# Optimization experiments

Measured on AMD Instinct MI355X. Metric: run time of the kernel, lower is better.

The kernel has to match this reference:

```python
import jax, jax.numpy as jnp
import numpy as np

N_POINTS = 200
LEVEL_DIM = 4
NUM_LEVELS = 3
RESOLUTIONS = (8, 16, 32)  # base_resolution=8, per-level scale 2
BATCH = 32768


def _sph_to_cart(theta, phi):
    st = jnp.sin(theta)
    return jnp.stack([st * jnp.cos(phi), st * jnp.sin(phi), jnp.cos(theta)], axis=-1)


def _sample_points(x):
    # x: [B,4] -> points on segment between two unit-sphere points: [B, N_POINTS, 3]
    p1 = _sph_to_cart(x[:, 0], x[:, 1])
    p2 = _sph_to_cart(x[:, 2], x[:, 3])
    t = jnp.linspace(0.0, 1.0, N_POINTS, dtype=x.dtype).reshape(1, N_POINTS, 1)
    return p1[:, None, :] + (p2 - p1)[:, None, :] * t


def _grid_interp(points, table, R):
    # points: [B,S,3] in [-1,1]; table: [(R+1)^3, D] dense grid. Trilinear interp.
    u = jnp.clip((points + 1.0) * 0.5, 0.0, 1.0) * R
    p0 = jnp.clip(jnp.floor(u).astype(jnp.int32), 0, R - 1)
    f = u - p0.astype(u.dtype)
    Rp1 = R + 1
    out = jnp.zeros(points.shape[:-1] + (table.shape[-1],), dtype=table.dtype)
    for c in range(8):  # fixed 8 trilinear corners
        off = np.array([(c >> 2) & 1, (c >> 1) & 1, c & 1], dtype=np.int32)
        idx = p0 + off
        lin = (idx[..., 0] * Rp1 + idx[..., 1]) * Rp1 + idx[..., 2]
        w = jnp.prod(jnp.where(off == 1, f, 1.0 - f), axis=-1)
        out = out + w[..., None] * table[lin]
    return out


def setup_inputs() -> dict:
    key = jax.random.key(0)
    ks = jax.random.split(key, 8)
    pi = 3.14159265
    x = jax.random.uniform(ks[0], (BATCH, 4), dtype=jnp.float32) * pi
    grid0 = jax.random.normal(ks[1], ((RESOLUTIONS[0] + 1) ** 3, LEVEL_DIM), jnp.float32) * 0.1
    grid1 = jax.random.normal(ks[2], ((RESOLUTIONS[1] + 1) ** 3, LEVEL_DIM), jnp.float32) * 0.1
    grid2 = jax.random.normal(ks[3], ((RESOLUTIONS[2] + 1) ** 3, LEVEL_DIM), jnp.float32) * 0.1
    w_label = jax.random.normal(ks[4], (NUM_LEVELS, 1), jnp.float32) * 0.5
    b_label = jnp.zeros((1,), jnp.float32)
    w_rgb = jax.random.normal(ks[5], (NUM_LEVELS * (LEVEL_DIM - 1), 3), jnp.float32) * 0.3
    b_rgb = jnp.zeros((3,), jnp.float32)
    return {"x": x, "grid0": grid0, "grid1": grid1, "grid2": grid2,
            "w_label": w_label, "b_label": b_label, "w_rgb": w_rgb, "b_rgb": b_rgb}


def reference(x, grid0, grid1, grid2, w_label, b_label, w_rgb, b_rgb):
    # torch wraps ray sampling in no_grad -> stop_gradient
    points = jax.lax.stop_gradient(_sample_points(x))  # [B,S,3]
    enc = jnp.concatenate(
        [_grid_interp(points, g, R) for g, R in zip((grid0, grid1, grid2), RESOLUTIONS)],
        axis=-1)  # [B,S,12]
    labels_in = enc[:, :, ::LEVEL_DIM]                      # [B,S,3]
    all_prob = jax.nn.sigmoid(labels_in @ w_label + b_label)  # [B,S,1]
    output_hits = jnp.max(all_prob, axis=1)                 # [B,1]
    mask = np.ones(NUM_LEVELS * LEVEL_DIM, dtype=bool)
    mask[::LEVEL_DIM] = False
    rgb_feats = enc[:, :, mask]                             # [B,S,9]
    hit = (all_prob > 0.5).astype(enc.dtype)
    idx_first = jnp.argmax(hit, axis=1)                     # [B,1] first sample with prob>0.5 (0 if none)
    idx3 = jnp.broadcast_to(idx_first[:, :, None], (rgb_feats.shape[0], 1, rgb_feats.shape[2]))
    gathered = jnp.take_along_axis(rgb_feats, idx3, axis=1)[:, 0, :]  # [B,9]
    output_rgb = jax.nn.sigmoid(gathered @ w_rgb + b_rgb)   # [B,3]
    return (output_hits, output_rgb)
```

## Files before the change

### kernel.cpp

```cpp
#include <hip/hip_runtime.h>
#include <math.h>

#define NPTS 200
#define L33   33
#define NLAT  35937
#define NPREP (NLAT * 4)

template<int R>
__device__ __forceinline__ float tri_label(const float* __restrict__ g,
                                           float ux, float uy, float uz) {
    constexpr int Rp1 = R + 1;
    constexpr int SX  = Rp1 * Rp1;
    int ix = min((int)ux, R - 1);
    int iy = min((int)uy, R - 1);
    int iz = min((int)uz, R - 1);
    float fx = ux - (float)ix, fy = uy - (float)iy, fz = uz - (float)iz;
    int b = (ix * Rp1 + iy) * Rp1 + iz;
    float v000 = g[4*b],            v001 = g[4*(b+1)];
    float v010 = g[4*(b+Rp1)],      v011 = g[4*(b+Rp1+1)];
    float v100 = g[4*(b+SX)],       v101 = g[4*(b+SX+1)];
    float v110 = g[4*(b+SX+Rp1)],   v111 = g[4*(b+SX+Rp1+1)];
    float c00 = fmaf(fz, v001 - v000, v000);
    float c01 = fmaf(fz, v011 - v010, v010);
    float c10 = fmaf(fz, v101 - v100, v100);
    float c11 = fmaf(fz, v111 - v110, v110);
    float c0  = fmaf(fy, c01 - c00, c00);
    float c1  = fmaf(fy, c11 - c10, c10);
    return fmaf(fx, c1 - c0, c0);
}

__global__ __launch_bounds__(256)
void prep_kernel(const float* __restrict__ g0, const float* __restrict__ g1,
                 const float* __restrict__ g2, const float* __restrict__ wl,
                 const float* __restrict__ bl, float* __restrict__ Pf) {
    int id = blockIdx.x * blockDim.x + threadIdx.x;
    if (id >= NPREP) return;
    int c  = id & 3;
    int jj = id >> 2;
    int ix = jj % L33;
    int r  = jj / L33;
    int iz = r % L33;
    int iy = r / L33;
    int jy = min(iy + (c >> 1), L33 - 1);
    int jz = min(iz + (c & 1),  L33 - 1);
    float fx = (float)ix, fy = (float)jy, fz = (float)jz;
    float L0 = tri_label<8 >(g0, fx * 0.25f, fy * 0.25f, fz * 0.25f);
    float L1 = tri_label<16>(g1, fx * 0.5f,  fy * 0.5f,  fz * 0.5f);
    float L2 = g2[4 * ((ix * L33 + jy) * L33 + jz)];
    Pf[id] = bl[0] + wl[0] * L0 + wl[1] * L1 + wl[2] * L2;
}

template<int R>
__device__ __forceinline__ void rgb_corner(const float* __restrict__ g,
                                           float cx, float cy, float cz,
                                           int dx, int dy, int dz,
                                           float* f3) {
    constexpr int Rp1 = R + 1;
    float ux = cx * (float)R, uy = cy * (float)R, uz = cz * (float)R;
    int ix = min((int)ux, R - 1);
    int iy = min((int)uy, R - 1);
    int iz = min((int)uz, R - 1);
    float fx = ux - (float)ix, fy = uy - (float)iy, fz = uz - (float)iz;
    int idx = ((ix + dx) * Rp1 + (iy + dy)) * Rp1 + (iz + dz);
    float w = (dx ? fx : 1.0f - fx) * (dy ? fy : 1.0f - fy) * (dz ? fz : 1.0f - fz);
    float4 v = *reinterpret_cast<const float4*>(g + 4 * idx);
    f3[0] = w * v.y;
    f3[1] = w * v.z;
    f3[2] = w * v.w;
}

__global__ __launch_bounds__(256, 4)
void rays_kernel(const float* __restrict__ x,
                 const float4* __restrict__ P,
                 const float* __restrict__ g0,
                 const float* __restrict__ g1,
                 const float* __restrict__ g2,
                 const float* __restrict__ wr,
                 const float* __restrict__ br,
                 float* __restrict__ out_hits,
                 float* __restrict__ out_rgb,
                 int n)
{
    const int tid = blockIdx.x * blockDim.x + threadIdx.x;
    const int ray = tid >> 4;
    const int sub = (int)(threadIdx.x & 15);
    if (ray >= n) return;

    const float th1 = x[ray * 4 + 0];
    const float ph1 = x[ray * 4 + 1];
    const float th2 = x[ray * 4 + 2];
    const float ph2 = x[ray * 4 + 3];
    float s1 = __sinf(th1), c1 = __cosf(th1);
    float s2 = __sinf(th2), c2 = __cosf(th2);
    float p1x = s1 * __cosf(ph1), p1y = s1 * __sinf(ph1), p1z = c1;
    float p2x = s2 * __cosf(ph2), p2y = s2 * __sinf(ph2), p2z = c2;
    const float dxr = p2x - p1x, dyr = p2y - p1y, dzr = p2z - p1z;

    const float inv = 1.0f / (float)(NPTS - 1);
    const float sc  = 16.0f * inv;

    const float bx = fmaf(p1x, 16.0f, 16.0f);
    const float by = fmaf(p1y, 16.0f, 16.0f);
    const float bz = fmaf(p1z, 16.0f, 16.0f);
    const float dux = dxr * sc, duy = dyr * sc, duz = dzr * sc;

    const float subf = (float)sub;
    float maxlogit = -INFINITY;
    unsigned hmask = 0u;

#define POINT_BODY(I)                                                          \
    {                                                                          \
        float tf = subf + (float)(16 * (I));             \
        float ux = fmaf(tf, dux, bx);                                          \
        float uy = fmaf(tf, duy, by);                                          \
        float uz = fmaf(tf, duz, bz);                                          \
        int ix = min((int)ux, 31);                                             \
        int iy = min((int)uy, 31);                                             \
        int iz = min((int)uz, 31);                                             \
        float fx = ux - (float)ix;                                             \
        float fy = uy - (float)iy;                                             \
        float fz = uz - (float)iz;                                             \
        int jj = (iy * L33 + iz) * L33 + ix;                                   \
        const float4* p = P + jj;                                              \
        float4 q0 = p[0];                                                      \
        float4 q1 = p[1];                                                      \
        float mx = fmaf(fx, q1.x - q0.x, q0.x);                                \
        float my = fmaf(fx, q1.y - q0.y, q0.y);                                \
        float mz = fmaf(fx, q1.z - q0.z, q0.z);                                \
        float mw = fmaf(fx, q1.w - q0.w, q0.w);                                \
        float r0 = fmaf(fz, my - mx, mx);                                      \
        float r1 = fmaf(fz, mw - mz, mz);                                      \
        float logit = fmaf(fy, r1 - r0, r0);                                   \
        maxlogit = fmaxf(maxlogit, logit);                                     \
        hmask |= (logit > 0.0f) ? (1u << (I)) : 0u;                            \
    }

#pragma unroll
    for (int i = 0; i < 12; ++i) POINT_BODY(i)
    if (sub < 8) POINT_BODY(12)
#undef POINT_BODY

    int fc = hmask ? (16 * __builtin_ctz(hmask) + sub) : NPTS;

#pragma unroll
    for (int m = 8; m >= 1; m >>= 1) {
        maxlogit = fmaxf(maxlogit, __shfl_xor(maxlogit, m, 64));
        fc = min(fc, __shfl_xor(fc, m, 64));
    }

    const int tsel = (fc >= NPTS) ? 0 : fc;
    {
        float tt = (float)tsel * inv;
        float px = fmaf(dxr, tt, p1x);
        float py = fmaf(dyr, tt, p1y);
        float pz = fmaf(dzr, tt, p1z);
        float cx = fminf(fmaxf(fmaf(px, 0.5f, 0.5f), 0.0f), 1.0f);
        float cy = fminf(fmaxf(fmaf(py, 0.5f, 0.5f), 0.0f), 1.0f);
        float cz = fminf(fmaxf(fmaf(pz, 0.5f, 0.5f), 0.0f), 1.0f);
        const int s8 = sub & 7;
        const int dx = (s8 >> 2) & 1, dy = (s8 >> 1) & 1, dz = s8 & 1;
        float feat[9];
        rgb_corner<8 >(g0, cx, cy, cz, dx, dy, dz, &feat[0]);
        rgb_corner<16>(g1, cx, cy, cz, dx, dy, dz, &feat[3]);
        rgb_corner<32>(g2, cx, cy, cz, dx, dy, dz, &feat[6]);
        float acc[3];
#pragma unroll
        for (int c = 0; c < 3; ++c) {
            float a = 0.0f;
#pragma unroll
            for (int f = 0; f < 9; ++f) a = fmaf(feat[f], wr[f * 3 + c], a);
            acc[c] = a;
        }
#pragma unroll
        for (int m = 4; m >= 1; m >>= 1) {
#pragma unroll
            for (int c = 0; c < 3; ++c)
                acc[c] += __shfl_xor(acc[c], m, 64);
        }
        if (sub == 0) {
            out_hits[ray] = 1.0f / (1.0f + __expf(-maxlogit));
#pragma unroll
            for (int c = 0; c < 3; ++c)
                out_rgb[ray * 3 + c] = 1.0f / (1.0f + __expf(-(acc[c] + br[c])));
        }
    }
}

extern "C" void kernel_launch(void* const* d_in, const int* in_sizes, int n_in,
                              void* d_out, int out_size, void* d_ws, size_t ws_size,
                              hipStream_t stream) {
    const float* x  = (const float*)d_in[0];
    const float* g0 = (const float*)d_in[1];
    const float* g1 = (const float*)d_in[2];
    const float* g2 = (const float*)d_in[3];
    const float* wl = (const float*)d_in[4];
    const float* bl = (const float*)d_in[5];
    const float* wr = (const float*)d_in[6];
    const float* br = (const float*)d_in[7];

    const int n = in_sizes[0] / 4;
    float* out_hits = (float*)d_out;
    float* out_rgb  = (float*)d_out + n;

    float* Pf = (float*)d_ws;

    prep_kernel<<<(NPREP + 255) / 256, 256, 0, stream>>>(g0, g1, g2, wl, bl, Pf);

    const int block = 256;
    const int grid = (n * 16 + block - 1) / block;
    rays_kernel<<<grid, block, 0, stream>>>(x, (const float4*)Pf, g0, g1, g2,
                                            wr, br, out_hits, out_rgb, n);
}
```

Baseline: 22.02 us.

## Pack per-cell label corners as bf16 with fp32 fallback near threshold

Replaces the two float4 loads per sample with one 16-byte load of all eight cell corners stored as bf16. A new pass builds a full fp32 label table, then a per-cell bf16 table and a global max-abs bound. Samples whose approximate logit falls within a tolerance band of zero are re-evaluated in fp32 to keep the first-hit index exact. This halves gather bandwidth per sample but adds an extra prep launch, an atomic, and a divergent fallback loop. The max logit (hence output_hits) is now taken from the bf16 values, so it is only approximate.

```diff
diff --git a/kernel.cpp b/kernel.cpp
--- a/kernel.cpp
+++ b/kernel.cpp
@@ -3,8 +3,12 @@
 
 #define NPTS 200
 #define L33   33
+#define L33SQ 1089
 #define NLAT  35937
-#define NPREP (NLAT * 4)
+#define NCELL 32768
+
+#define WS_T_OFF_BYTES   (NCELL * 16)
+#define WS_THR_OFF_BYTES (WS_T_OFF_BYTES + NLAT * 4)
 
 template<int R>
 __device__ __forceinline__ float tri_label(const float* __restrict__ g,
@@ -30,24 +34,56 @@
 }
 
 __global__ __launch_bounds__(256)
-void prep_kernel(const float* __restrict__ g0, const float* __restrict__ g1,
-                 const float* __restrict__ g2, const float* __restrict__ wl,
-                 const float* __restrict__ bl, float* __restrict__ Pf) {
-    int id = blockIdx.x * blockDim.x + threadIdx.x;
-    if (id >= NPREP) return;
-    int c  = id & 3;
-    int jj = id >> 2;
-    int ix = jj % L33;
-    int r  = jj / L33;
-    int iz = r % L33;
-    int iy = r / L33;
-    int jy = min(iy + (c >> 1), L33 - 1);
-    int jz = min(iz + (c & 1),  L33 - 1);
-    float fx = (float)ix, fy = (float)jy, fz = (float)jz;
+void prep1_kernel(const float* __restrict__ g0, const float* __restrict__ g1,
+                  const float* __restrict__ g2, const float* __restrict__ wl,
+                  const float* __restrict__ bl, float* __restrict__ T,
+                  unsigned* __restrict__ thrU) {
+    int i = blockIdx.x * blockDim.x + threadIdx.x;
+    if (i == 0) *thrU = 0u;
+    if (i >= NLAT) return;
+    int jz = i % L33;
+    int r  = i / L33;
+    int jy = r % L33;
+    int jx = r / L33;
+    float fx = (float)jx, fy = (float)jy, fz = (float)jz;
     float L0 = tri_label<8 >(g0, fx * 0.25f, fy * 0.25f, fz * 0.25f);
     float L1 = tri_label<16>(g1, fx * 0.5f,  fy * 0.5f,  fz * 0.5f);
-    float L2 = g2[4 * ((ix * L33 + jy) * L33 + jz)];
-    Pf[id] = bl[0] + wl[0] * L0 + wl[1] * L1 + wl[2] * L2;
+    float L2 = g2[4 * i];
+    T[i] = bl[0] + wl[0] * L0 + wl[1] * L1 + wl[2] * L2;
+}
+
+__device__ __forceinline__ unsigned bf16_rne(float v) {
+    unsigned u = __float_as_uint(v);
+    return u + 0x7fffu + ((u >> 16) & 1u);
+}
+
+__global__ __launch_bounds__(256)
+void prep2_kernel(const float* __restrict__ T, uint4* __restrict__ H,
+                  unsigned* __restrict__ thrU) {
+    int cell = blockIdx.x * blockDim.x + threadIdx.x;
+    int ix = cell & 31;
+    int iz = (cell >> 5) & 31;
+    int iy = cell >> 10;
+    int b = (ix * L33 + iy) * L33 + iz;
+    float v000 = T[b],              v001 = T[b + 1];
+    float v010 = T[b + L33],        v011 = T[b + L33 + 1];
+    float v100 = T[b + L33SQ],      v101 = T[b + L33SQ + 1];
+    float v110 = T[b + L33SQ + L33],v111 = T[b + L33SQ + L33 + 1];
+    uint4 o;
+    o.x = (bf16_rne(v000) >> 16) | (bf16_rne(v001) & 0xffff0000u);
+    o.y = (bf16_rne(v010) >> 16) | (bf16_rne(v011) & 0xffff0000u);
+    o.z = (bf16_rne(v100) >> 16) | (bf16_rne(v101) & 0xffff0000u);
+    o.w = (bf16_rne(v110) >> 16) | (bf16_rne(v111) & 0xffff0000u);
+    H[cell] = o;
+    float ma = fmaxf(fmaxf(fmaxf(fabsf(v000), fabsf(v001)),
+                           fmaxf(fabsf(v010), fabsf(v011))),
+                     fmaxf(fmaxf(fabsf(v100), fabsf(v101)),
+                           fmaxf(fabsf(v110), fabsf(v111))));
+#pragma unroll
+    for (int m = 32; m >= 1; m >>= 1)
+        ma = fmaxf(ma, __shfl_xor(ma, m, 64));
+    if ((threadIdx.x & 63) == 0)
+        atomicMax(thrU, __float_as_uint(ma));
 }
 
 template<int R>
@@ -71,7 +107,9 @@
 
 __global__ __launch_bounds__(256, 4)
 void rays_kernel(const float* __restrict__ x,
-                 const float4* __restrict__ P,
+                 const uint4* __restrict__ H,
+                 const float* __restrict__ T,
+                 const unsigned* __restrict__ thrU,
                  const float* __restrict__ g0,
                  const float* __restrict__ g1,
                  const float* __restrict__ g2,
@@ -86,6 +124,9 @@
     const int sub = (int)(threadIdx.x & 15);
     if (ray >= n) return;
 
+    const float maxAbs = __uint_as_float(*thrU);
+    const float thrG = fmaf(4e-3f, maxAbs, 1e-5f);
+
     const float th1 = x[ray * 4 + 0];
     const float ph1 = x[ray * 4 + 1];
     const float th2 = x[ray * 4 + 2];
@@ -107,6 +148,7 @@
     const float subf = (float)sub;
     float maxlogit = -INFINITY;
     unsigned hmask = 0u;
+    unsigned smask = 0u;
 
 #define POINT_BODY(I)                                                          \
     {                                                                          \
@@ -120,19 +162,27 @@
         float fx = ux - (float)ix;                                             \
         float fy = uy - (float)iy;                                             \
         float fz = uz - (float)iz;                                             \
-        int jj = (iy * L33 + iz) * L33 + ix;                                   \
-        const float4* p = P + jj;                                              \
-        float4 q0 = p[0];                                                      \
-        float4 q1 = p[1];                                                      \
-        float mx = fmaf(fx, q1.x - q0.x, q0.x);                                \
-        float my = fmaf(fx, q1.y - q0.y, q0.y);                                \
-        float mz = fmaf(fx, q1.z - q0.z, q0.z);                                \
-        float mw = fmaf(fx, q1.w - q0.w, q0.w);                                \
-        float r0 = fmaf(fz, my - mx, mx);                                      \
-        float r1 = fmaf(fz, mw - mz, mz);                                      \
+        int cell = (iy << 10) | (iz << 5) | ix;                                \
+        uint4 raw = H[cell];                                                   \
+        float c000 = __uint_as_float(raw.x << 16);                             \
+        float c001 = __uint_as_float(raw.x & 0xffff0000u);                     \
+        float c010 = __uint_as_float(raw.y << 16);                             \
+        float c011 = __uint_as_float(raw.y & 0xffff0000u);                     \
+        float c100 = __uint_as_float(raw.z << 16);                             \
+        float c101 = __uint_as_float(raw.z & 0xffff0000u);                     \
+        float c110 = __uint_as_float(raw.w << 16);                             \
+        float c111 = __uint_as_float(raw.w & 0xffff0000u);                     \
+        float b00 = fmaf(fx, c100 - c000, c000);                               \
+        float b01 = fmaf(fx, c101 - c001, c001);                               \
+        float b10 = fmaf(fx, c110 - c010, c010);                               \
+        float b11 = fmaf(fx, c111 - c011, c011);                               \
+        float r0 = fmaf(fz, b01 - b00, b00);                                   \
+        float r1 = fmaf(fz, b11 - b10, b10);                                   \
         float logit = fmaf(fy, r1 - r0, r0);                                   \
         maxlogit = fmaxf(maxlogit, logit);                                     \
-        hmask |= (logit > 0.0f) ? (1u << (I)) : 0u;                            \
+        unsigned bit = 1u << (I);                                              \
+        hmask |= (logit > thrG)         ? bit : 0u;                            \
+        smask |= (fabsf(logit) <= thrG) ? bit : 0u;                            \
     }
 
 #pragma unroll
@@ -148,7 +198,43 @@
         fc = min(fc, __shfl_xor(fc, m, 64));
     }
 
-    const int tsel = (fc >= NPTS) ? 0 : fc;
+    int fh = fc;
+    unsigned mm = smask;
+    while (mm) {
+        int i = __builtin_ctz(mm);
+        mm &= mm - 1;
+        int t = 16 * i + sub;
+        if (t >= fh) break;
+        float tf = (float)t;
+        float ux = fmaf(tf, dux, bx);
+        float uy = fmaf(tf, duy, by);
+        float uz = fmaf(tf, duz, bz);
+        int ix = min((int)ux, 31);
+        int iy = min((int)uy, 31);
+        int iz = min((int)uz, 31);
+        float fx = ux - (float)ix;
+        float fy = uy - (float)iy;
+        float fz = uz - (float)iz;
+        int b = (ix * L33 + iy) * L33 + iz;
+        float v000 = T[b],               v001 = T[b + 1];
+        float v010 = T[b + L33],         v011 = T[b + L33 + 1];
+        float v100 = T[b + L33SQ],       v101 = T[b + L33SQ + 1];
+        float v110 = T[b + L33SQ + L33], v111 = T[b + L33SQ + L33 + 1];
+        float b00 = fmaf(fx, v100 - v000, v000);
+        float b01 = fmaf(fx, v101 - v001, v001);
+        float b10 = fmaf(fx, v110 - v010, v010);
+        float b11 = fmaf(fx, v111 - v011, v011);
+        float r0 = fmaf(fz, b01 - b00, b00);
+        float r1 = fmaf(fz, b11 - b10, b10);
+        float lg = fmaf(fy, r1 - r0, r0);
+        if (lg > 0.0f) { fh = t; break; }
+    }
+
+#pragma unroll
+    for (int m = 8; m >= 1; m >>= 1)
+        fh = min(fh, __shfl_xor(fh, m, 64));
+
+    const int tsel = (fh >= NPTS) ? 0 : fh;
     {
         float tt = (float)tsel * inv;
         float px = fmaf(dxr, tt, p1x);
@@ -202,12 +288,15 @@
     float* out_hits = (float*)d_out;
     float* out_rgb  = (float*)d_out + n;
 
-    float* Pf = (float*)d_ws;
-
-    prep_kernel<<<(NPREP + 255) / 256, 256, 0, stream>>>(g0, g1, g2, wl, bl, Pf);
+    uint4*    H    = (uint4*)d_ws;
+    float*    T    = (float*)((char*)d_ws + WS_T_OFF_BYTES);
+    unsigned* thrU = (unsigned*)((char*)d_ws + WS_THR_OFF_BYTES);
+
+    prep1_kernel<<<(NLAT + 255) / 256, 256, 0, stream>>>(g0, g1, g2, wl, bl, T, thrU);
+    prep2_kernel<<<NCELL / 256, 256, 0, stream>>>(T, H, thrU);
 
     const int block = 256;
     const int grid = (n * 16 + block - 1) / block;
-    rays_kernel<<<grid, block, 0, stream>>>(x, (const float4*)Pf, g0, g1, g2,
+    rays_kernel<<<grid, block, 0, stream>>>(x, H, T, thrU, g0, g1, g2,
                                             wr, br, out_hits, out_rgb, n);
 }
```

After: 31.43 us. 42.7% more time.
